# Optimization experiments

Measured on AMD Instinct MI355X. Metric: run time of the kernel, lower is better.

Reference implementation:

```python
import jax, jax.numpy as jnp
import numpy as np

T, A = 2048, 64          # n_thread, n_agents
RAWOB, N_TP, N_GP = 120, 5, 2
E = N_TP * N_GP          # number of sub-nets (type x group placeholder)
D = RAWOB + N_TP + 1     # augmented obs dim fed to each Net
H = 128                  # hidden width of each sub-net MLP
N_ACTION = 16


def setup_inputs() -> dict:
    key = jax.random.key(0)
    ks = jax.random.split(key, 12)
    s1 = 1.0 / np.sqrt(D)
    s2 = 1.0 / np.sqrt(H)
    return {
        "obs": jax.random.normal(ks[0], (T, A, RAWOB), dtype=jnp.float32),
        "hete_pick": jax.random.randint(ks[1], (T, A), 0, E),
        "hete_type": jax.random.randint(ks[2], (T, A), 0, N_TP),
        "gp_sel_summary": jax.random.randint(ks[3], (T, N_TP), 0, N_GP),
        # per-expert actor MLP params [E, ...]
        "W1": jax.random.normal(ks[4], (E, D, H), dtype=jnp.float32) * s1,
        "b1": jnp.zeros((E, H), dtype=jnp.float32),
        "W2": jax.random.normal(ks[5], (E, H, N_ACTION), dtype=jnp.float32) * s2,
        "b2": jnp.zeros((E, N_ACTION), dtype=jnp.float32),
        # central critic params
        "Wc1": jax.random.normal(ks[6], (D, H), dtype=jnp.float32) * s1,
        "bc1": jnp.zeros((H,), dtype=jnp.float32),
        "Wc2": jax.random.normal(ks[7], (H, 1), dtype=jnp.float32) * s2,
        "bc2": jnp.zeros((1,), dtype=jnp.float32),
    }


def _augment_obs(obs, hete_type, gp_sel_summary):
    # obs <- cat(obs, hete_type, gp_sel_summary with -1 scattered at own type idx)
    t, a, _ = obs.shape
    n_tp = gp_sel_summary.shape[1]
    gp = jnp.broadcast_to(gp_sel_summary[:, None, :].astype(obs.dtype), (t, a, n_tp))
    oh = jax.nn.one_hot(hete_type, n_tp, dtype=obs.dtype)
    gp_obs = gp * (1.0 - oh) - oh  # scatter -1 at index hete_type
    return jnp.concatenate([obs, hete_type[..., None].astype(obs.dtype), gp_obs], axis=-1)


def reference(obs, hete_pick, hete_type, gp_sel_summary,
              W1, b1, W2, b2, Wc1, bc1, Wc2, bc2):
    t, a, _ = obs.shape
    x = _augment_obs(obs, hete_type, gp_sel_summary)          # [T, A, D]
    xf = x.reshape(t * a, -1)                                  # [N, D]
    pick = hete_pick.reshape(t * a)                            # [N]
    n_exp = W1.shape[0]
    # dispatch: each token routed to exactly one sub-net; dense compute + masked combine
    logits = jnp.zeros((t * a, W2.shape[-1]), dtype=obs.dtype)
    for e in range(n_exp):  # small fixed expert loop
        y = jax.nn.relu(xf @ W1[e] + b1[e]) @ W2[e] + b2[e]    # [N, n_action]
        logits = jnp.where((pick == e)[:, None], y, logits)
    logits = logits.reshape(t, a, -1)
    # central critic on all tokens
    value = (jax.nn.relu(xf @ Wc1 + bc1) @ Wc2 + bc2).reshape(t, a, 1)
    return logits, value
```

## Files before the change

kernel.cpp:

```cpp
#include <hip/hip_runtime.h>
#include <hip/hip_bf16.h>

#define T_DIM   2048
#define A_DIM   64
#define N_TOK   (T_DIM * A_DIM)
#define RAWOB   120
#define N_TP    5
#define E_EXP   10
#define D_DIM   126
#define DP      128
#define H_DIM   128
#define N_ACT   16
#define BTOK    256
#define NBLK    (N_TOK / BTOK)
#define LOGITS_SZ (N_TOK * N_ACT)

typedef __bf16 bh8 __attribute__((ext_vector_type(8)));
typedef ushort u16x8 __attribute__((ext_vector_type(8)));
typedef ushort u16x4 __attribute__((ext_vector_type(4)));
typedef short  s16x4 __attribute__((ext_vector_type(4)));
typedef float  f32x4 __attribute__((ext_vector_type(4)));

__device__ __forceinline__ f32x4 mfma16(bh8 a, bh8 b, f32x4 c) {
    return __builtin_amdgcn_mfma_f32_16x16x32_bf16(a, b, c, 0, 0, 0);
}
__device__ __forceinline__ f32x4 mfma16k16(s16x4 a, s16x4 b, f32x4 c) {
    return __builtin_amdgcn_mfma_f32_16x16x16bf16_1k(a, b, c, 0, 0, 0);
}

__device__ __forceinline__ ushort f2bf(float f) {
    unsigned x = __builtin_bit_cast(unsigned, f);
    unsigned r = (x + 0x7fffu + ((x >> 16) & 1u)) >> 16;
    return (ushort)r;
}

#define W1P_N (E_EXP * H_DIM * DP)
#define W2P_N (E_EXP * N_ACT * H_DIM)
#define WC1P_N (DP * DP)

#define PB_BLOCKS 124

__global__ __launch_bounds__(256) void prep_kernel(
    const float* __restrict__ W1, const float* __restrict__ W2,
    const float* __restrict__ Wc1, const float* __restrict__ b1,
    const float* __restrict__ bc1,
    ushort* __restrict__ W1p, ushort* __restrict__ W2p, ushort* __restrict__ Wc1p)
{
    int bx = blockIdx.x, tid = threadIdx.x;
    if (bx < 44) {
        __shared__ ushort st[32][130];
        const float* src;
        const float* bias;
        ushort* dstbase;
        int kt;
        if (bx < 40) {
            int e = bx >> 2;
            kt = bx & 3;
            src = W1 + (e * D_DIM + kt * 32) * H_DIM;
            bias = b1 + e * H_DIM;
            dstbase = W1p + e * (H_DIM * DP);
        } else {
            kt = bx - 40;
            src = Wc1 + kt * 32 * H_DIM;
            bias = bc1;
            dstbase = Wc1p;
        }
        int dmax = D_DIM - kt * 32;
#pragma unroll
        for (int p = 0; p < 16; ++p) {
            int idx = p * 256 + tid;
            int dd = idx >> 7, n = idx & 127;
            float v;
            if (dd < dmax)                    v = src[dd * H_DIM + n];
            else if (kt == 3 && dd == 30)     v = bias[n];
            else                              v = 0.f;
            st[dd][n] = f2bf(v);
        }
        __syncthreads();
#pragma unroll
        for (int p = 0; p < 16; ++p) {
            int idx = p * 256 + tid;
            int dd = idx >> 7, n = idx & 127;
            dstbase[((n >> 4) * 4 + kt) * 512 + ((dd >> 3) * 16 + (n & 15)) * 8 + (dd & 7)]
                = st[dd][n];
        }
    } else {
        int i = (bx - 44) * 256 + tid;
        int e   = i >> 11;
        int rem = i & 2047;
        int kk  = rem >> 8;
        int idx = rem & 255;
        int l = idx >> 2, j = idx & 3;
        int lq = l >> 4, lm = l & 15;
        W2p[i] = f2bf(W2[(e * H_DIM + kk * 16 + lq * 4 + j) * N_ACT + lm]);
    }
}

__global__ __launch_bounds__(512, 4) void moe_kernel(
    const float* __restrict__ obs, const int* __restrict__ pick,
    const int* __restrict__ hete_type, const int* __restrict__ gp_sel,
    const float* __restrict__ b2, const float* __restrict__ bc2,
    const ushort* __restrict__ W1p, const ushort* __restrict__ W2p,
    const ushort* __restrict__ Wc1p, const float* __restrict__ Wc2,
    float* __restrict__ out)
{
    __shared__ __align__(16) ushort xa[BTOK * 128];
    __shared__ short map[576];
    __shared__ short jexp[24];
    __shared__ short jtb[24];
    __shared__ int lc[16], lbase[16];
    __shared__ int nj_tot;

    const int bx  = blockIdx.x;
    const int tid = threadIdx.x;
    const int gbase = bx * BTOK;

    if (tid < 16) lc[tid] = 0;
    for (int i = tid; i < 576; i += 512) map[i] = -1;
    __syncthreads();

    int mye = 0, myloc = 0;
    if (tid < BTOK) {
        mye = pick[gbase + tid];
        myloc = atomicAdd(&lc[mye], 1);
    }

#pragma unroll
    for (int p = 0; p < 8; ++p) {
        int idx = p * 512 + tid;
        if (idx < BTOK * 15) {
            int r = idx / 15, g = idx - r * 15;
            const float* s = obs + (size_t)(gbase + r) * RAWOB + g * 8;
            float4 u0 = *(const float4*)(const void*)s;
            float4 u1 = *(const float4*)(const void*)(s + 4);
            u16x8 t;
            t[0] = f2bf(u0.x); t[1] = f2bf(u0.y); t[2] = f2bf(u0.z); t[3] = f2bf(u0.w);
            t[4] = f2bf(u1.x); t[5] = f2bf(u1.y); t[6] = f2bf(u1.z); t[7] = f2bf(u1.w);
            *(u16x8*)(void*)(xa + r * 128 + (g ^ (r & 15)) * 8) = t;
        }
    }
    if (tid < BTOK) {
        int tok = gbase + tid;
        int ht = hete_type[tok];
        int tt = tok >> 6;
        u16x8 t;
        t[0] = f2bf((float)ht);
#pragma unroll
        for (int q = 0; q < N_TP; ++q) {
            float g = (q == ht) ? -1.0f : (float)gp_sel[tt * N_TP + q];
            t[1 + q] = f2bf(g);
        }
        t[6] = (ushort)0x3F80;
        t[7] = 0;
        *(u16x8*)(void*)(xa + tid * 128 + (15 ^ (tid & 15)) * 8) = t;
    }
    __syncthreads();

    if (tid == 0) {
        int pb = 0, nj = 0;
#pragma unroll
        for (int e = 0; e < E_EXP; ++e) {
            lbase[e] = pb;
            int ntile = (lc[e] + 15) >> 4;
            int npair = (ntile + 1) >> 1;
            for (int k = 0; k < npair; ++k) {
                jexp[nj] = (short)e;
                jtb[nj]  = (short)(pb + k * 32);
                ++nj;
            }
            pb += npair * 32;
        }
        nj_tot = nj;
    }
    __syncthreads();
    if (tid < BTOK) map[lbase[mye] + myloc] = (short)tid;
    __syncthreads();

    const int w = tid >> 6;
    const int l = tid & 63;
    const int lm = l & 15;
    const int lq = l >> 4;
    const float bcv = bc2[0];

    const int NJ = nj_tot;
    for (int i = w; i < NJ; i += 8) {
        const int e  = jexp[i];
        const int tb = jtb[i];
        const int m0 = map[tb + lm];
        const int m1 = map[tb + 16 + lm];
        const int row0 = m0 < 0 ? 0 : m0;
        const int row1 = m1 < 0 ? 0 : m1;
        bh8 a0[4], a1[4];
#pragma unroll
        for (int kt = 0; kt < 4; ++kt) {
            int g = kt * 4 + lq;
            a0[kt] = *(const bh8*)(const void*)(xa + row0 * 128 + (g ^ (row0 & 15)) * 8);
            a1[kt] = *(const bh8*)(const void*)(xa + row1 * 128 + (g ^ (row1 & 15)) * 8);
        }
        const ushort* w1e = W1p + e * (H_DIM * DP);
        const ushort* w2e = W2p + e * 2048;
        const float bb = b2[e * N_ACT + lm];
        f32x4 y0 = (f32x4){0.f, 0.f, 0.f, 0.f};
        f32x4 y1 = (f32x4){0.f, 0.f, 0.f, 0.f};
#pragma unroll
        for (int nt = 0; nt < 8; ++nt) {
            f32x4 ae0 = (f32x4){0.f, 0.f, 0.f, 0.f}, ae1 = ae0;
#pragma unroll
            for (int kt = 0; kt < 4; ++kt) {
                bh8 wf = *(const bh8*)(const void*)(w1e + (nt * 4 + kt) * 512 + l * 8);
                ae0 = mfma16(wf, a0[kt], ae0);
                ae1 = mfma16(wf, a1[kt], ae1);
            }
            u16x4 hp0, hp1;
#pragma unroll
            for (int r = 0; r < 4; ++r) {
                hp0[r] = f2bf(fmaxf(ae0[r], 0.f));
                hp1[r] = f2bf(fmaxf(ae1[r], 0.f));
            }
            s16x4 w2f = *(const s16x4*)(const void*)(w2e + nt * 256 + l * 4);
            y0 = mfma16k16(__builtin_bit_cast(s16x4, hp0), w2f, y0);
            y1 = mfma16k16(__builtin_bit_cast(s16x4, hp1), w2f, y1);
        }
#pragma unroll
        for (int r = 0; r < 4; ++r) {
            int s0 = map[tb + lq * 4 + r];
            if (s0 >= 0) out[(size_t)(gbase + s0) * N_ACT + lm] = y0[r] + bb;
            int s1 = map[tb + 16 + lq * 4 + r];
            if (s1 >= 0) out[(size_t)(gbase + s1) * N_ACT + lm] = y1[r] + bb;
        }
    }

    {
        const int r0 = w * 32;
        const int row0 = r0 + lm, row1 = r0 + 16 + lm;
        bh8 a0[4], a1[4];
#pragma unroll
        for (int kt = 0; kt < 4; ++kt) {
            int g = kt * 4 + lq;
            a0[kt] = *(const bh8*)(const void*)(xa + row0 * 128 + (g ^ (row0 & 15)) * 8);
            a1[kt] = *(const bh8*)(const void*)(xa + row1 * 128 + (g ^ (row1 & 15)) * 8);
        }
        float p0 = 0.f, p1 = 0.f;
#pragma unroll
        for (int nt = 0; nt < 8; ++nt) {
            f32x4 c0 = (f32x4){0.f,0.f,0.f,0.f}, c1 = c0;
#pragma unroll
            for (int kt = 0; kt < 4; ++kt) {
                bh8 wf = *(const bh8*)(const void*)(Wc1p + (nt * 4 + kt) * 512 + l * 8);
                c0 = mfma16(wf, a0[kt], c0);
                c1 = mfma16(wf, a1[kt], c1);
            }
            const float4 wc = *(const float4*)(const void*)(Wc2 + nt * 16 + lq * 4);
            p0 += fmaxf(c0[0], 0.f) * wc.x + fmaxf(c0[1], 0.f) * wc.y
                + fmaxf(c0[2], 0.f) * wc.z + fmaxf(c0[3], 0.f) * wc.w;
            p1 += fmaxf(c1[0], 0.f) * wc.x + fmaxf(c1[1], 0.f) * wc.y
                + fmaxf(c1[2], 0.f) * wc.z + fmaxf(c1[3], 0.f) * wc.w;
        }
        p0 += __shfl_xor(p0, 16, 64); p0 += __shfl_xor(p0, 32, 64);
        p1 += __shfl_xor(p1, 16, 64); p1 += __shfl_xor(p1, 32, 64);
        if (lq == 0) {
            out[LOGITS_SZ + gbase + row0] = p0 + bcv;
            out[LOGITS_SZ + gbase + row1] = p1 + bcv;
        }
    }
}

extern "C" void kernel_launch(void* const* d_in, const int* in_sizes, int n_in,
                              void* d_out, int out_size, void* d_ws, size_t ws_size,
                              hipStream_t stream) {
    const float* obs  = (const float*)d_in[0];
    const int*   pick = (const int*)d_in[1];
    const int*   htyp = (const int*)d_in[2];
    const int*   gp   = (const int*)d_in[3];
    const float* W1   = (const float*)d_in[4];
    const float* b1   = (const float*)d_in[5];
    const float* W2   = (const float*)d_in[6];
    const float* b2   = (const float*)d_in[7];
    const float* Wc1  = (const float*)d_in[8];
    const float* bc1  = (const float*)d_in[9];
    const float* Wc2  = (const float*)d_in[10];
    const float* bc2  = (const float*)d_in[11];
    float* out = (float*)d_out;

    ushort* W1p  = (ushort*)d_ws;
    ushort* W2p  = W1p + W1P_N;
    ushort* Wc1p = W2p + W2P_N;

    prep_kernel<<<PB_BLOCKS, 256, 0, stream>>>(
        W1, W2, Wc1, b1, bc1, W1p, W2p, Wc1p);
    moe_kernel<<<NBLK, 512, 0, stream>>>(
        obs, pick, htyp, gp, b2, bc2,
        W1p, W2p, Wc1p, Wc2, out);
}
```

Before: 131.6 us.

## Prefetch W1 fragments, split MFMA chains, and compute job schedule per thread

Removes the single-thread job-list build and its extra barrier; every thread now derives expert offsets and job indices from shared counts in registers. The expert and critic GEMM loops double-buffer the next weight fragments from global memory, hiding load latency behind the current MFMAs. The four-deep MFMA accumulation chain is split into two independent chains that are summed afterwards, which shortens the dependency chain. The cost is more register pressure under launch_bounds(512,4) and a small per-job scalar search over ten experts.

```diff
diff --git a/kernel.cpp b/kernel.cpp
--- a/kernel.cpp
+++ b/kernel.cpp
@@ -96,6 +96,8 @@
     }
 }
 
+#define NPAIR(c) (((((c) + 15) >> 4) + 1) >> 1)
+
 __global__ __launch_bounds__(512, 4) void moe_kernel(
     const float* __restrict__ obs, const int* __restrict__ pick,
     const int* __restrict__ hete_type, const int* __restrict__ gp_sel,
@@ -106,10 +108,7 @@
 {
     __shared__ __align__(16) ushort xa[BTOK * 128];
     __shared__ short map[576];
-    __shared__ short jexp[24];
-    __shared__ short jtb[24];
-    __shared__ int lc[16], lbase[16];
-    __shared__ int nj_tot;
+    __shared__ int lc[16];
 
     const int bx  = blockIdx.x;
     const int tid = threadIdx.x;
@@ -156,24 +155,16 @@
     }
     __syncthreads();
 
-    if (tid == 0) {
-        int pb = 0, nj = 0;
-#pragma unroll
-        for (int e = 0; e < E_EXP; ++e) {
-            lbase[e] = pb;
-            int ntile = (lc[e] + 15) >> 4;
-            int npair = (ntile + 1) >> 1;
-            for (int k = 0; k < npair; ++k) {
-                jexp[nj] = (short)e;
-                jtb[nj]  = (short)(pb + k * 32);
-                ++nj;
-            }
-            pb += npair * 32;
-        }
-        nj_tot = nj;
-    }
-    __syncthreads();
-    if (tid < BTOK) map[lbase[mye] + myloc] = (short)tid;
+    int cnt[10], np[10];
+#pragma unroll
+    for (int e = 0; e < E_EXP; ++e) { cnt[e] = lc[e]; np[e] = NPAIR(cnt[e]); }
+    int lb = 0;
+#pragma unroll
+    for (int e = 0; e < E_EXP - 1; ++e) lb += (mye > e) ? np[e] * 32 : 0;
+    if (tid < BTOK) map[lb + myloc] = (short)tid;
+    int NJ = 0;
+#pragma unroll
+    for (int e = 0; e < E_EXP; ++e) NJ += np[e];
     __syncthreads();
 
     const int w = tid >> 6;
@@ -182,10 +173,15 @@
     const int lq = l >> 4;
     const float bcv = bc2[0];
 
-    const int NJ = nj_tot;
     for (int i = w; i < NJ; i += 8) {
-        const int e  = jexp[i];
-        const int tb = jtb[i];
+        int e = 0, tb = 0, pj = 0, ps = 0;
+#pragma unroll
+        for (int q = 0; q < E_EXP; ++q) {
+            bool hit = (i >= pj) && (i < pj + np[q]);
+            if (hit) { e = q; tb = ps + (i - pj) * 32; }
+            pj += np[q];
+            ps += np[q] * 32;
+        }
         const int m0 = map[tb + lm];
         const int m1 = map[tb + 16 + lm];
         const int row0 = m0 < 0 ? 0 : m0;
@@ -202,15 +198,26 @@
         const float bb = b2[e * N_ACT + lm];
         f32x4 y0 = (f32x4){0.f, 0.f, 0.f, 0.f};
         f32x4 y1 = (f32x4){0.f, 0.f, 0.f, 0.f};
+        bh8 wf0 = *(const bh8*)(const void*)(w1e + 0 * 512 + l * 8);
+        bh8 wf1 = *(const bh8*)(const void*)(w1e + 1 * 512 + l * 8);
+        bh8 wf2 = *(const bh8*)(const void*)(w1e + 2 * 512 + l * 8);
+        bh8 wf3 = *(const bh8*)(const void*)(w1e + 3 * 512 + l * 8);
 #pragma unroll
         for (int nt = 0; nt < 8; ++nt) {
-            f32x4 ae0 = (f32x4){0.f, 0.f, 0.f, 0.f}, ae1 = ae0;
-#pragma unroll
-            for (int kt = 0; kt < 4; ++kt) {
-                bh8 wf = *(const bh8*)(const void*)(w1e + (nt * 4 + kt) * 512 + l * 8);
-                ae0 = mfma16(wf, a0[kt], ae0);
-                ae1 = mfma16(wf, a1[kt], ae1);
+            bh8 nf0 = wf0, nf1 = wf1, nf2 = wf2, nf3 = wf3;
+            if (nt < 7) {
+                nf0 = *(const bh8*)(const void*)(w1e + ((nt + 1) * 4 + 0) * 512 + l * 8);
+                nf1 = *(const bh8*)(const void*)(w1e + ((nt + 1) * 4 + 1) * 512 + l * 8);
+                nf2 = *(const bh8*)(const void*)(w1e + ((nt + 1) * 4 + 2) * 512 + l * 8);
+                nf3 = *(const bh8*)(const void*)(w1e + ((nt + 1) * 4 + 3) * 512 + l * 8);
             }
+            f32x4 z = (f32x4){0.f, 0.f, 0.f, 0.f};
+            f32x4 p0a = mfma16(wf0, a0[0], z), p0b = mfma16(wf2, a0[2], z);
+            f32x4 p1a = mfma16(wf0, a1[0], z), p1b = mfma16(wf2, a1[2], z);
+            p0a = mfma16(wf1, a0[1], p0a);  p0b = mfma16(wf3, a0[3], p0b);
+            p1a = mfma16(wf1, a1[1], p1a);  p1b = mfma16(wf3, a1[3], p1b);
+            f32x4 ae0 = p0a + p0b;
+            f32x4 ae1 = p1a + p1b;
             u16x4 hp0, hp1;
 #pragma unroll
             for (int r = 0; r < 4; ++r) {
@@ -220,6 +227,7 @@
             s16x4 w2f = *(const s16x4*)(const void*)(w2e + nt * 256 + l * 4);
             y0 = mfma16k16(__builtin_bit_cast(s16x4, hp0), w2f, y0);
             y1 = mfma16k16(__builtin_bit_cast(s16x4, hp1), w2f, y1);
+            wf0 = nf0; wf1 = nf1; wf2 = nf2; wf3 = nf3;
         }
 #pragma unroll
         for (int r = 0; r < 4; ++r) {
@@ -241,20 +249,32 @@
             a1[kt] = *(const bh8*)(const void*)(xa + row1 * 128 + (g ^ (row1 & 15)) * 8);
         }
         float p0 = 0.f, p1 = 0.f;
+        bh8 wf0 = *(const bh8*)(const void*)(Wc1p + 0 * 512 + l * 8);
+        bh8 wf1 = *(const bh8*)(const void*)(Wc1p + 1 * 512 + l * 8);
+        bh8 wf2 = *(const bh8*)(const void*)(Wc1p + 2 * 512 + l * 8);
+        bh8 wf3 = *(const bh8*)(const void*)(Wc1p + 3 * 512 + l * 8);
 #pragma unroll
         for (int nt = 0; nt < 8; ++nt) {
-            f32x4 c0 = (f32x4){0.f,0.f,0.f,0.f}, c1 = c0;
-#pragma unroll
-            for (int kt = 0; kt < 4; ++kt) {
-                bh8 wf = *(const bh8*)(const void*)(Wc1p + (nt * 4 + kt) * 512 + l * 8);
-                c0 = mfma16(wf, a0[kt], c0);
-                c1 = mfma16(wf, a1[kt], c1);
+            bh8 nf0 = wf0, nf1 = wf1, nf2 = wf2, nf3 = wf3;
+            if (nt < 7) {
+                nf0 = *(const bh8*)(const void*)(Wc1p + ((nt + 1) * 4 + 0) * 512 + l * 8);
+                nf1 = *(const bh8*)(const void*)(Wc1p + ((nt + 1) * 4 + 1) * 512 + l * 8);
+                nf2 = *(const bh8*)(const void*)(Wc1p + ((nt + 1) * 4 + 2) * 512 + l * 8);
+                nf3 = *(const bh8*)(const void*)(Wc1p + ((nt + 1) * 4 + 3) * 512 + l * 8);
             }
+            f32x4 z = (f32x4){0.f, 0.f, 0.f, 0.f};
+            f32x4 c0a = mfma16(wf0, a0[0], z), c0b = mfma16(wf2, a0[2], z);
+            f32x4 c1a = mfma16(wf0, a1[0], z), c1b = mfma16(wf2, a1[2], z);
+            c0a = mfma16(wf1, a0[1], c0a);  c0b = mfma16(wf3, a0[3], c0b);
+            c1a = mfma16(wf1, a1[1], c1a);  c1b = mfma16(wf3, a1[3], c1b);
+            f32x4 c0 = c0a + c0b;
+            f32x4 c1 = c1a + c1b;
             const float4 wc = *(const float4*)(const void*)(Wc2 + nt * 16 + lq * 4);
             p0 += fmaxf(c0[0], 0.f) * wc.x + fmaxf(c0[1], 0.f) * wc.y
                 + fmaxf(c0[2], 0.f) * wc.z + fmaxf(c0[3], 0.f) * wc.w;
             p1 += fmaxf(c1[0], 0.f) * wc.x + fmaxf(c1[1], 0.f) * wc.y
                 + fmaxf(c1[2], 0.f) * wc.z + fmaxf(c1[3], 0.f) * wc.w;
+            wf0 = nf0; wf1 = nf1; wf2 = nf2; wf3 = nf3;
         }
         p0 += __shfl_xor(p0, 16, 64); p0 += __shfl_xor(p0, 32, 64);
         p1 += __shfl_xor(p1, 16, 64); p1 += __shfl_xor(p1, 32, 64);
```

Result: slower. 136.8 us (+3.9%).
